# Optimization experiments

Hardware: AMD Instinct MI355X
Metric: run time of the kernel (lower is better)

Reference implementation:

```python
import jax, jax.numpy as jnp
import numpy as np

N_NODES = 50000
N_EDGES = 800000
D = 64            # NODE_FEATURE_DIM == EDGE_FEATURE_DIM
H = 128           # EDGE_FEATURE_HIDDEN
EDGE_STEPS = 4
NODE_STEPS = 2


def _mlp2(h, W1, b1, W2, b2):
    # two-layer MLP with ReLU between (bn=False, end_with_relu=False)
    return jnp.maximum(h @ W1 + b1, 0.0) @ W2 + b2


def setup_inputs() -> dict:
    key = jax.random.key(0)
    ks = iter(jax.random.split(key, 40))

    def w(shape):
        fan_in = shape[0]
        return jax.random.normal(next(ks), shape, dtype=jnp.float32) / np.sqrt(fan_in)

    inp = {
        "x": jax.random.normal(next(ks), (N_NODES, 128), dtype=jnp.float32),
        "edge_attr": jax.random.normal(next(ks), (N_EDGES, 19), dtype=jnp.float32),
        "edge_index": jax.random.randint(next(ks), (2, N_EDGES), 0, N_NODES),
        "node_types": jax.random.randint(next(ks), (N_NODES,), 0, 17),
        # node embedding MLP: 128 -> 64 -> 64
        "ne_W1": w((128, D)), "ne_b1": jnp.zeros((D,)), "ne_W2": w((D, D)), "ne_b2": jnp.zeros((D,)),
        # edge embedding MLP: 19 -> 64 -> 64
        "ee_W1": w((19, D)), "ee_b1": jnp.zeros((D,)), "ee_W2": w((D, D)), "ee_b2": jnp.zeros((D,)),
        # MPN edge MLP: [x_src(2D), x_dst(2D), e(2D)] = 384 -> 128 -> 64
        "mp_eW1": w((6 * D, H)), "mp_eb1": jnp.zeros((H,)), "mp_eW2": w((H, D)), "mp_eb2": jnp.zeros((D,)),
        # MPN node-update MLP: 64 -> 64
        "mp_nW": w((D, D)), "mp_nb": jnp.zeros((D,)),
        # edge classification head: 64 -> 32 -> 1
        "ec_W1": w((D, 32)), "ec_b1": jnp.zeros((32,)), "ec_W2": w((32, 1)), "ec_b2": jnp.zeros((1,)),
        # node classification head: 64 -> 32 -> 1
        "nc_W1": w((D, 32)), "nc_b1": jnp.zeros((32,)), "nc_W2": w((32, 1)), "nc_b2": jnp.zeros((1,)),
        # type classification head: 64 -> 32 -> 17
        "cl_W1": w((D, 32)), "cl_b1": jnp.zeros((32,)), "cl_W2": w((32, 17)), "cl_b2": jnp.zeros((17,)),
    }
    return inp


def reference(x, edge_attr, edge_index, node_types,
              ne_W1, ne_b1, ne_W2, ne_b2,
              ee_W1, ee_b1, ee_W2, ee_b2,
              mp_eW1, mp_eb1, mp_eW2, mp_eb2,
              mp_nW, mp_nb,
              ec_W1, ec_b1, ec_W2, ec_b2,
              nc_W1, nc_b1, nc_W2, nc_b2,
              cl_W1, cl_b1, cl_W2, cl_b2):
    src, dst = edge_index[0], edge_index[1]

    nf0 = _mlp2(x, ne_W1, ne_b1, ne_W2, ne_b2)          # [N, D] initial node emb
    ef0 = _mlp2(edge_attr, ee_W1, ee_b1, ee_W2, ee_b2)  # [E, D] initial edge emb
    nf, ef = nf0, ef0

    def mpn_step(nf, ef):
        # skip connections: concat initial features each iteration
        nf_c = jnp.concatenate([nf0, nf], axis=1)   # [N, 2D]
        ef_c = jnp.concatenate([ef0, ef], axis=1)   # [E, 2D]
        msg_in = jnp.concatenate([nf_c[src], nf_c[dst], ef_c], axis=1)  # [E, 6D]
        e_new = _mlp2(msg_in, mp_eW1, mp_eb1, mp_eW2, mp_eb2)           # [E, D]
        agg = jax.ops.segment_sum(e_new, dst, num_segments=N_NODES)    # [N, D]
        n_new = jnp.maximum(agg @ mp_nW + mp_nb, 0.0)                   # [N, D]
        return n_new, e_new

    for _ in range(EDGE_STEPS):
        nf, ef = mpn_step(nf, ef)
    pred_edge = _mlp2(ef, ec_W1, ec_b1, ec_W2, ec_b2).squeeze(-1)  # [E]

    for _ in range(NODE_STEPS):
        nf, ef = mpn_step(nf, ef)
    pred_node = _mlp2(nf, nc_W1, nc_b1, nc_W2, nc_b2).squeeze(-1)  # [N]
    pred_class = _mlp2(nf, cl_W1, cl_b1, cl_W2, cl_b2)             # [N, 17]

    return (pred_edge, pred_node, pred_class)
```

## Files before the change

kernel.cpp:

```cpp
#include <hip/hip_runtime.h>

#define NN 50000
#define EE 800000

typedef unsigned short u16;
typedef __attribute__((ext_vector_type(8))) short bf16x8;
typedef __attribute__((ext_vector_type(4))) float f32x4;

#define MFMA16(a, b, c) __builtin_amdgcn_mfma_f32_16x16x32_bf16(a, b, c, 0, 0, 0)

__device__ __forceinline__ float bf2f(u16 v) {
    union { unsigned u; float f; } x; x.u = ((unsigned)v) << 16; return x.f;
}
__device__ __forceinline__ u16 f2bf(float f) {
    union { float f; unsigned u; } x; x.f = f;
    unsigned r = x.u + 0x7FFFu + ((x.u >> 16) & 1u);
    return (u16)(r >> 16);
}
__device__ __forceinline__ void gl_lds16(const u16* g, u16* l) {
    __builtin_amdgcn_global_load_lds((const __attribute__((address_space(1))) void*)g,
                                     (__attribute__((address_space(3))) void*)l, 16, 0, 0);
}

__global__ void pack_frag(const float* __restrict__ W, u16* __restrict__ dst, int K, int N) {
    int i = blockIdx.x * 256 + threadIdx.x;
    int nfc = N / 16, kkc = (K + 31) / 32;
    int total = kkc * nfc * 512;
    if (i >= total) return;
    int t = i & 7, lane = (i >> 3) & 63;
    int rest = i >> 9;
    int nf = rest % nfc, kk = rest / nfc;
    int k = kk * 32 + (lane >> 4) * 8 + t, n = nf * 16 + (lane & 15);
    dst[i] = (k < K) ? f2bf(W[k * N + n]) : (u16)0;
}

__global__ __launch_bounds__(256) void embed_mfma_node(
    const float* __restrict__ x, const u16* __restrict__ pW1, const float* __restrict__ b1,
    const u16* __restrict__ pW2, const float* __restrict__ b2, u16* __restrict__ out)
{
    __shared__ alignas(16) u16 A[64 * 136];
    __shared__ alignas(16) u16 Hs[64 * 72];
    int tid = threadIdx.x;
    size_t row0 = (size_t)blockIdx.x * 64;
    #pragma unroll
    for (int it = 0; it < 8; ++it) {
        int u = it * 256 + tid;
        int row = u >> 5, seg = u & 31;
        float4 v = (row0 + row < NN) ? *(const float4*)(x + (row0 + row) * 128 + seg * 4)
                                     : make_float4(0.f, 0.f, 0.f, 0.f);
        ushort4 o; o.x = f2bf(v.x); o.y = f2bf(v.y); o.z = f2bf(v.z); o.w = f2bf(v.w);
        *(ushort4*)(A + row * 136 + seg * 4) = o;
    }
    __syncthreads();
    int wave = tid >> 6, lane = tid & 63, l15 = lane & 15, l4 = lane >> 4;
    int col = wave * 16 + l15;
    f32x4 acc[4] = {};
    #pragma unroll
    for (int kk = 0; kk < 4; ++kk) {
        bf16x8 b = *(const bf16x8*)(pW1 + (size_t)((kk * 4 + wave) * 64 + lane) * 8);
        #pragma unroll
        for (int mi = 0; mi < 4; ++mi) {
            bf16x8 a = *(const bf16x8*)(A + (mi * 16 + l15) * 136 + kk * 32 + l4 * 8);
            acc[mi] = MFMA16(a, b, acc[mi]);
        }
    }
    float bias = b1[col];
    #pragma unroll
    for (int mi = 0; mi < 4; ++mi)
        #pragma unroll
        for (int r = 0; r < 4; ++r) {
            float v = acc[mi][r] + bias;
            Hs[(mi * 16 + l4 * 4 + r) * 72 + col] = f2bf(v > 0.f ? v : 0.f);
        }
    __syncthreads();
    f32x4 acc2[4] = {};
    #pragma unroll
    for (int kk = 0; kk < 2; ++kk) {
        bf16x8 b = *(const bf16x8*)(pW2 + (size_t)((kk * 4 + wave) * 64 + lane) * 8);
        #pragma unroll
        for (int mi = 0; mi < 4; ++mi) {
            bf16x8 a = *(const bf16x8*)(Hs + (mi * 16 + l15) * 72 + kk * 32 + l4 * 8);
            acc2[mi] = MFMA16(a, b, acc2[mi]);
        }
    }
    float bias2 = b2[col];
    __syncthreads();
    #pragma unroll
    for (int mi = 0; mi < 4; ++mi)
        #pragma unroll
        for (int r = 0; r < 4; ++r)
            Hs[(mi * 16 + l4 * 4 + r) * 72 + col] = f2bf(acc2[mi][r] + bias2);
    __syncthreads();
    #pragma unroll
    for (int it = 0; it < 4; ++it) {
        int u = it * 256 + tid;
        int row = u >> 4, c4 = (u & 15) * 4;
        if (row0 + row < NN) {
            ushort4 o = *(const ushort4*)(Hs + row * 72 + c4);
            *(ushort4*)(out + (row0 + row) * 64 + c4) = o;
        }
    }
}

__global__ __launch_bounds__(256) void embed_mfma_edge(
    const float* __restrict__ ea, const u16* __restrict__ pW1, const float* __restrict__ b1,
    const u16* __restrict__ pW2, const float* __restrict__ b2, u16* __restrict__ out)
{
    __shared__ alignas(16) u16 A[64 * 40];
    __shared__ alignas(16) u16 Hs[64 * 72];
    int tid = threadIdx.x;
    size_t row0 = (size_t)blockIdx.x * 64;
    #pragma unroll
    for (int it = 0; it < 8; ++it) {
        int u = it * 256 + tid;
        int row = u >> 5, k = u & 31;
        float v = (k < 19) ? ea[(row0 + row) * 19 + k] : 0.f;
        A[row * 40 + k] = f2bf(v);
    }
    __syncthreads();
    int wave = tid >> 6, lane = tid & 63, l15 = lane & 15, l4 = lane >> 4;
    int col = wave * 16 + l15;
    f32x4 acc[4] = {};
    {
        bf16x8 b = *(const bf16x8*)(pW1 + (size_t)(wave * 64 + lane) * 8);
        #pragma unroll
        for (int mi = 0; mi < 4; ++mi) {
            bf16x8 a = *(const bf16x8*)(A + (mi * 16 + l15) * 40 + l4 * 8);
            acc[mi] = MFMA16(a, b, acc[mi]);
        }
    }
    float bias = b1[col];
    #pragma unroll
    for (int mi = 0; mi < 4; ++mi)
        #pragma unroll
        for (int r = 0; r < 4; ++r) {
            float v = acc[mi][r] + bias;
            Hs[(mi * 16 + l4 * 4 + r) * 72 + col] = f2bf(v > 0.f ? v : 0.f);
        }
    __syncthreads();
    f32x4 acc2[4] = {};
    #pragma unroll
    for (int kk = 0; kk < 2; ++kk) {
        bf16x8 b = *(const bf16x8*)(pW2 + (size_t)((kk * 4 + wave) * 64 + lane) * 8);
        #pragma unroll
        for (int mi = 0; mi < 4; ++mi) {
            bf16x8 a = *(const bf16x8*)(Hs + (mi * 16 + l15) * 72 + kk * 32 + l4 * 8);
            acc2[mi] = MFMA16(a, b, acc2[mi]);
        }
    }
    float bias2 = b2[col];
    __syncthreads();
    #pragma unroll
    for (int mi = 0; mi < 4; ++mi)
        #pragma unroll
        for (int r = 0; r < 4; ++r)
            Hs[(mi * 16 + l4 * 4 + r) * 72 + col] = f2bf(acc2[mi][r] + bias2);
    __syncthreads();
    #pragma unroll
    for (int it = 0; it < 4; ++it) {
        int u = it * 256 + tid;
        int row = u >> 4, c4 = (u & 15) * 4;
        ushort4 o = *(const ushort4*)(Hs + row * 72 + c4);
        *(ushort4*)(out + (row0 + row) * 64 + c4) = o;
    }
}

__global__ void zero_cnt(int* __restrict__ cnt) {
    int i = blockIdx.x * 256 + threadIdx.x;
    if (i < NN) cnt[i] = 0;
}
__global__ void count_deg(const int* __restrict__ eidx, int* __restrict__ cnt) {
    int e = blockIdx.x * 256 + threadIdx.x;
    if (e < EE) atomicAdd(&cnt[eidx[EE + e]], 1);
}
__global__ void scan_k(const int* __restrict__ cnt, int* __restrict__ starts) {
    __shared__ int part[1024];
    int t = threadIdx.x;
    const int chunk = (NN + 1023) / 1024;
    int lo = t * chunk, hi = lo + chunk; if (hi > NN) hi = NN;
    if (lo > NN) lo = NN;
    int s = 0;
    for (int i = lo; i < hi; ++i) s += cnt[i];
    part[t] = s;
    __syncthreads();
    for (int off = 1; off < 1024; off <<= 1) {
        int v = part[t];
        int add = (t >= off) ? part[t - off] : 0;
        __syncthreads();
        part[t] = v + add;
        __syncthreads();
    }
    int run = (t == 0) ? 0 : part[t - 1];
    for (int i = lo; i < hi; ++i) { starts[i] = run; run += cnt[i]; }
    if (t == 1023) starts[NN] = EE;
}
__global__ void init_cur(const int* __restrict__ starts, int* __restrict__ cur) {
    int i = blockIdx.x * 256 + threadIdx.x;
    if (i < NN) cur[i] = starts[i];
}
__global__ void scatter_e(const int* __restrict__ eidx, int* __restrict__ cur,
                          int* __restrict__ eids) {
    int e = blockIdx.x * 256 + threadIdx.x;
    if (e < EE) {
        int pos = atomicAdd(&cur[eidx[EE + e]], 1);
        eids[pos] = e;
    }
}

__global__ __launch_bounds__(256, 3) void edge_mlp(
    const int* __restrict__ eidx,
    const u16* __restrict__ nf0, const u16* __restrict__ nfc,
    const u16* __restrict__ ef0, const u16* __restrict__ efc,
    const u16* __restrict__ pW1, const u16* __restrict__ pW2,
    const float* __restrict__ eb1, const float* __restrict__ eb2,
    u16* __restrict__ efn)
{
    __shared__ alignas(16) u16 Chunk[6][64 * 64];
    const int tid = threadIdx.x;
    const int tile0 = blockIdx.x * 64;
    const int wave = tid >> 6, lane = tid & 63;
    const int l15 = lane & 15, l4 = lane >> 4;

    const int r0 = wave * 16 + (lane >> 3);
    const int r1 = r0 + 8;
    const int u_ = lane & 7;
    const int su0 = u_ ^ (r0 & 7);
    const int su1 = u_ ^ (r1 & 7);
    const int is0 = eidx[tile0 + r0] * 64;
    const int is1 = eidx[tile0 + r1] * 64;
    const int id0 = eidx[EE + tile0 + r0] * 64;
    const int id1 = eidx[EE + tile0 + r1] * 64;

    bf16x8 bw[24];
    #pragma unroll
    for (int kk = 0; kk < 12; ++kk) {
        bw[kk * 2 + 0] = *(const bf16x8*)(pW1 + (size_t)((kk * 8 + wave * 2 + 0) * 64 + lane) * 8);
        bw[kk * 2 + 1] = *(const bf16x8*)(pW1 + (size_t)((kk * 8 + wave * 2 + 1) * 64 + lane) * 8);
    }
    __builtin_amdgcn_sched_barrier(0);

    #pragma unroll
    for (int c = 0; c < 6; ++c) {
        const u16 *b0, *b1;
        if (c == 0)      { b0 = nf0 + is0; b1 = nf0 + is1; }
        else if (c == 1) { b0 = nfc + is0; b1 = nfc + is1; }
        else if (c == 2) { b0 = nf0 + id0; b1 = nf0 + id1; }
        else if (c == 3) { b0 = nfc + id0; b1 = nfc + id1; }
        else if (c == 4) { b0 = ef0 + (size_t)(tile0 + r0) * 64; b1 = ef0 + (size_t)(tile0 + r1) * 64; }
        else             { b0 = efc + (size_t)(tile0 + r0) * 64; b1 = efc + (size_t)(tile0 + r1) * 64; }
        u16* l0 = (u16*)Chunk + c * 4096 + wave * 1024;
        gl_lds16(b0 + su0 * 8, l0);
        gl_lds16(b1 + su1 * 8, l0 + 512);
    }
    __builtin_amdgcn_sched_barrier(0);

    f32x4 acc[4][2] = {};
    #pragma unroll
    for (int c = 0; c < 6; ++c) {
        if (c == 0)      asm volatile("s_waitcnt vmcnt(10)" ::: "memory");
        else if (c == 1) asm volatile("s_waitcnt vmcnt(8)" ::: "memory");
        else if (c == 2) asm volatile("s_waitcnt vmcnt(6)" ::: "memory");
        else if (c == 3) asm volatile("s_waitcnt vmcnt(4)" ::: "memory");
        else if (c == 4) asm volatile("s_waitcnt vmcnt(2)" ::: "memory");
        else             asm volatile("s_waitcnt vmcnt(0)" ::: "memory");
        __builtin_amdgcn_s_barrier();
        __builtin_amdgcn_sched_barrier(0);
        const char* Cb = (const char*)Chunk + c * 8192;
        #pragma unroll
        for (int kkl = 0; kkl < 2; ++kkl) {
            const int kk = c * 2 + kkl;
            #pragma unroll
            for (int mi = 0; mi < 4; ++mi) {
                int row = mi * 16 + l15;
                bf16x8 a = *(const bf16x8*)(Cb + row * 128 + ((kkl * 64 + l4 * 16) ^ ((row & 7) << 4)));
                acc[mi][0] = MFMA16(a, bw[kk * 2 + 0], acc[mi][0]);
                acc[mi][1] = MFMA16(a, bw[kk * 2 + 1], acc[mi][1]);
            }
        }
    }

    char* HidB = (char*)Chunk;
    #pragma unroll
    for (int nj = 0; nj < 2; ++nj) {
        int col = wave * 32 + nj * 16 + l15;
        float bias = eb1[col];
        #pragma unroll
        for (int mi = 0; mi < 4; ++mi) {
            #pragma unroll
            for (int r = 0; r < 4; ++r) {
                int row = mi * 16 + l4 * 4 + r;
                float v = acc[mi][nj][r] + bias;
                v = v > 0.f ? v : 0.f;
                *(u16*)(HidB + row * 256 + ((col * 2) ^ ((row & 7) << 4))) = f2bf(v);
            }
        }
    }
    __syncthreads();

    f32x4 acc2[4] = {};
    const int m0 = wave * 16;
    #pragma unroll
    for (int kk = 0; kk < 4; ++kk) {
        int row = m0 + l15;
        bf16x8 a = *(const bf16x8*)(HidB + row * 256 + ((kk * 64 + l4 * 16) ^ ((row & 7) << 4)));
        #pragma unroll
        for (int nf = 0; nf < 4; ++nf) {
            bf16x8 b = *(const bf16x8*)(pW2 + (size_t)((kk * 4 + nf) * 64 + lane) * 8);
            acc2[nf] = MFMA16(a, b, acc2[nf]);
        }
    }

    float* EnF = (float*)((char*)Chunk + 16384);
    #pragma unroll
    for (int nf = 0; nf < 4; ++nf) {
        int col = nf * 16 + l15;
        float bias = eb2[col];
        #pragma unroll
        for (int r = 0; r < 4; ++r) {
            int row = m0 + l4 * 4 + r;
            EnF[row * 64 + col] = acc2[nf][r] + bias;
        }
    }
    __syncthreads();
    #pragma unroll
    for (int rep = 0; rep < 4; ++rep) {
        int u = rep * 256 + tid;
        int el = u >> 4, d0 = (u & 15) * 4;
        const float* s = EnF + el * 64 + d0;
        ushort4 o;
        o.x = f2bf(s[0]); o.y = f2bf(s[1]); o.z = f2bf(s[2]); o.w = f2bf(s[3]);
        *(ushort4*)(efn + (size_t)(tile0 + el) * 64 + d0) = o;
    }
}

__global__ __launch_bounds__(256) void node_update(
    const u16* __restrict__ enew,
    const int* __restrict__ starts, const int* __restrict__ eids,
    const float* __restrict__ Wn, const float* __restrict__ bn,
    u16* __restrict__ nfn)
{
    __shared__ float Wns[64 * 64];
    int tid = threadIdx.x;
    for (int i = tid; i < 4096; i += 256) Wns[i] = Wn[i];
    __syncthreads();
    int w = tid >> 6, l = tid & 63, g = l >> 4, q = l & 15;
    int nbase = blockIdx.x * 64 + w * 16;
    float bnl = bn[l];
    for (int ni = 0; ni < 16; ++ni) {
        int n = nbase + ni;
        if (n >= NN) break;
        int s0 = starts[n], s1 = starts[n + 1];
        float a0 = 0.f, a1 = 0.f, a2 = 0.f, a3 = 0.f;
        for (int j0 = s0; j0 < s1; j0 += 4) {
            int j = j0 + g;
            if (j < s1) {
                int e = eids[j];
                ushort4 v = *(const ushort4*)(enew + (size_t)e * 64 + q * 4);
                a0 += bf2f(v.x); a1 += bf2f(v.y); a2 += bf2f(v.z); a3 += bf2f(v.w);
            }
        }
        a0 += __shfl_xor(a0, 16); a0 += __shfl_xor(a0, 32);
        a1 += __shfl_xor(a1, 16); a1 += __shfl_xor(a1, 32);
        a2 += __shfl_xor(a2, 16); a2 += __shfl_xor(a2, 32);
        a3 += __shfl_xor(a3, 16); a3 += __shfl_xor(a3, 32);
        float o = bnl;
        #pragma unroll
        for (int hq = 0; hq < 16; ++hq) {
            float b0 = __shfl(a0, hq), b1 = __shfl(a1, hq);
            float b2 = __shfl(a2, hq), b3 = __shfl(a3, hq);
            o += b0 * Wns[(hq * 4 + 0) * 64 + l];
            o += b1 * Wns[(hq * 4 + 1) * 64 + l];
            o += b2 * Wns[(hq * 4 + 2) * 64 + l];
            o += b3 * Wns[(hq * 4 + 3) * 64 + l];
        }
        o = o > 0.f ? o : 0.f;
        nfn[(size_t)n * 64 + l] = f2bf(o);
    }
}

__global__ __launch_bounds__(256) void edge_head(
    const u16* __restrict__ ef, const u16* __restrict__ pW1, const float* __restrict__ b1,
    const float* __restrict__ W2, const float* __restrict__ b2, float* __restrict__ out)
{
    __shared__ alignas(16) u16 A[64 * 72];
    int tid = threadIdx.x;
    int tile0 = blockIdx.x * 64;
    #pragma unroll
    for (int it = 0; it < 2; ++it) {
        int u = it * 256 + tid;
        int row = u >> 3, sub = u & 7;
        uint4 v = *(const uint4*)(ef + (size_t)(tile0 + row) * 64 + sub * 8);
        *(uint4*)(A + row * 72 + sub * 8) = v;
    }
    __syncthreads();
    int wave = tid >> 6, lane = tid & 63, l15 = lane & 15, l4 = lane >> 4;
    int m0 = wave * 16;
    f32x4 acc[2] = {};
    #pragma unroll
    for (int kk = 0; kk < 2; ++kk) {
        bf16x8 a = *(const bf16x8*)(A + (m0 + l15) * 72 + kk * 32 + l4 * 8);
        #pragma unroll
        for (int nf = 0; nf < 2; ++nf) {
            bf16x8 b = *(const bf16x8*)(pW1 + (size_t)((kk * 2 + nf) * 64 + lane) * 8);
            acc[nf] = MFMA16(a, b, acc[nf]);
        }
    }
    float bias2 = b2[0];
    #pragma unroll
    for (int r = 0; r < 4; ++r) {
        float p = 0.f;
        #pragma unroll
        for (int nf = 0; nf < 2; ++nf) {
            int col = nf * 16 + l15;
            float h = acc[nf][r] + b1[col];
            p += (h > 0.f ? h : 0.f) * W2[col];
        }
        p += __shfl_xor(p, 1); p += __shfl_xor(p, 2);
        p += __shfl_xor(p, 4); p += __shfl_xor(p, 8);
        if (l15 == 0) out[tile0 + m0 + l4 * 4 + r] = p + bias2;
    }
}

__global__ void node_head(const u16* __restrict__ nf,
                          const float* __restrict__ ncW1, const float* __restrict__ ncb1,
                          const float* __restrict__ ncW2, const float* __restrict__ ncb2,
                          const float* __restrict__ clW1, const float* __restrict__ clb1,
                          const float* __restrict__ clW2, const float* __restrict__ clb2,
                          float* __restrict__ outN, float* __restrict__ outC) {
    __shared__ float sNW1[2048], sCW1[2048], sCW2[32 * 17];
    __shared__ float sNb1[32], sCb1[32], sNW2[32], sCb2[17];
    int tid = threadIdx.x;
    for (int i = tid; i < 2048; i += 256) { sNW1[i] = ncW1[i]; sCW1[i] = clW1[i]; }
    for (int i = tid; i < 544; i += 256) sCW2[i] = clW2[i];
    if (tid < 32) { sNb1[tid] = ncb1[tid]; sCb1[tid] = clb1[tid]; sNW2[tid] = ncW2[tid]; }
    if (tid < 17) sCb2[tid] = clb2[tid];
    __syncthreads();
    int n = blockIdx.x * 256 + tid;
    if (n >= NN) return;
    const u16* r = nf + (size_t)n * 64;
    float v[64];
    for (int k4 = 0; k4 < 16; ++k4) {
        ushort4 q = *(const ushort4*)(r + k4 * 4);
        v[k4 * 4 + 0] = bf2f(q.x); v[k4 * 4 + 1] = bf2f(q.y);
        v[k4 * 4 + 2] = bf2f(q.z); v[k4 * 4 + 3] = bf2f(q.w);
    }
    float h[32];
    #pragma unroll
    for (int j = 0; j < 32; ++j) h[j] = sNb1[j];
    for (int k = 0; k < 64; ++k) {
        float vk = v[k];
        #pragma unroll
        for (int j = 0; j < 32; ++j) h[j] += vk * sNW1[k * 32 + j];
    }
    float o = ncb2[0];
    #pragma unroll
    for (int j = 0; j < 32; ++j) o += (h[j] > 0.f ? h[j] : 0.f) * sNW2[j];
    outN[n] = o;
    #pragma unroll
    for (int j = 0; j < 32; ++j) h[j] = sCb1[j];
    for (int k = 0; k < 64; ++k) {
        float vk = v[k];
        #pragma unroll
        for (int j = 0; j < 32; ++j) h[j] += vk * sCW1[k * 32 + j];
    }
    float oc[17];
    #pragma unroll
    for (int c = 0; c < 17; ++c) oc[c] = sCb2[c];
    #pragma unroll
    for (int j = 0; j < 32; ++j) {
        float hr = h[j] > 0.f ? h[j] : 0.f;
        #pragma unroll
        for (int c = 0; c < 17; ++c) oc[c] += hr * sCW2[j * 17 + c];
    }
    #pragma unroll
    for (int c = 0; c < 17; ++c) outC[(size_t)n * 17 + c] = oc[c];
}

extern "C" void kernel_launch(void* const* d_in, const int* in_sizes, int n_in,
                              void* d_out, int out_size, void* d_ws, size_t ws_size,
                              hipStream_t stream) {
    const float* x     = (const float*)d_in[0];
    const float* ea    = (const float*)d_in[1];
    const int*   eidx  = (const int*)d_in[2];
    const float* neW1  = (const float*)d_in[4];
    const float* neb1  = (const float*)d_in[5];
    const float* neW2  = (const float*)d_in[6];
    const float* neb2  = (const float*)d_in[7];
    const float* eeW1  = (const float*)d_in[8];
    const float* eeb1  = (const float*)d_in[9];
    const float* eeW2  = (const float*)d_in[10];
    const float* eeb2  = (const float*)d_in[11];
    const float* mpW1  = (const float*)d_in[12];
    const float* mpb1  = (const float*)d_in[13];
    const float* mpW2  = (const float*)d_in[14];
    const float* mpb2  = (const float*)d_in[15];
    const float* mpnW  = (const float*)d_in[16];
    const float* mpnb  = (const float*)d_in[17];
    const float* ecW1  = (const float*)d_in[18];
    const float* ecb1  = (const float*)d_in[19];
    const float* ecW2  = (const float*)d_in[20];
    const float* ecb2  = (const float*)d_in[21];
    const float* ncW1  = (const float*)d_in[22];
    const float* ncb1  = (const float*)d_in[23];
    const float* ncW2  = (const float*)d_in[24];
    const float* ncb2  = (const float*)d_in[25];
    const float* clW1  = (const float*)d_in[26];
    const float* clb1  = (const float*)d_in[27];
    const float* clW2  = (const float*)d_in[28];
    const float* clb2  = (const float*)d_in[29];

    char* w = (char*)d_ws;
    size_t used = 0;
    auto alloc = [&](size_t b) {
        char* p = w + used; used += (b + 255) & ~(size_t)255; return p;
    };
    u16* nf0  = (u16*)alloc((size_t)NN * 64 * 2);
    u16* nfW  = (u16*)alloc((size_t)NN * 64 * 2);
    u16* ef0  = (u16*)alloc((size_t)EE * 64 * 2);
    u16* efW  = (u16*)alloc((size_t)EE * 64 * 2);
    u16* pmW1 = (u16*)alloc(49152 * 2);
    u16* pmW2 = (u16*)alloc(8192 * 2);
    u16* pnW1 = (u16*)alloc(8192 * 2);
    u16* pnW2 = (u16*)alloc(4096 * 2);
    u16* peW1 = (u16*)alloc(2048 * 2);
    u16* peW2 = (u16*)alloc(4096 * 2);
    u16* pcW1 = (u16*)alloc(2048 * 2);
    int* cnt    = (int*)alloc((size_t)NN * 4);
    int* starts = (int*)alloc((size_t)(NN + 1) * 4);
    int* eids   = (int*)alloc((size_t)EE * 4);
    if (used > ws_size) return;

    pack_frag<<<192, 256, 0, stream>>>(mpW1, pmW1, 384, 128);
    pack_frag<<<32, 256, 0, stream>>>(mpW2, pmW2, 128, 64);
    pack_frag<<<32, 256, 0, stream>>>(neW1, pnW1, 128, 64);
    pack_frag<<<16, 256, 0, stream>>>(neW2, pnW2, 64, 64);
    pack_frag<<<8, 256, 0, stream>>>(eeW1, peW1, 19, 64);
    pack_frag<<<16, 256, 0, stream>>>(eeW2, peW2, 64, 64);
    pack_frag<<<8, 256, 0, stream>>>(ecW1, pcW1, 64, 32);

    embed_mfma_node<<<(NN + 63) / 64, 256, 0, stream>>>(x, pnW1, neb1, pnW2, neb2, nf0);
    embed_mfma_edge<<<EE / 64, 256, 0, stream>>>(ea, peW1, eeb1, peW2, eeb2, ef0);

    zero_cnt<<<(NN + 255) / 256, 256, 0, stream>>>(cnt);
    count_deg<<<EE / 256, 256, 0, stream>>>(eidx, cnt);
    scan_k<<<1, 1024, 0, stream>>>(cnt, starts);
    init_cur<<<(NN + 255) / 256, 256, 0, stream>>>(starts, cnt);
    scatter_e<<<EE / 256, 256, 0, stream>>>(eidx, cnt, eids);

    float* outE = (float*)d_out;
    float* outN = outE + EE;
    float* outC = outN + NN;

    const u16* nfc = nf0;
    const u16* efc = ef0;
    for (int s = 0; s < 6; ++s) {
        edge_mlp<<<EE / 64, 256, 0, stream>>>(eidx, nf0, nfc, ef0, efc, pmW1, pmW2, mpb1, mpb2, efW);
        node_update<<<(NN + 63) / 64, 256, 0, stream>>>(efW, starts, eids, mpnW, mpnb, nfW);
        if (s == 3)
            edge_head<<<EE / 64, 256, 0, stream>>>(efW, pcW1, ecb1, ecW2, ecb2, outE);
        efc = efW;
        nfc = nfW;
    }
    node_head<<<(NN + 255) / 256, 256, 0, stream>>>(nfc, ncW1, ncb1, ncW2, ncb2,
                                                    clW1, clb1, clW2, clb2, outN, outC);
    (void)in_sizes; (void)n_in; (void)out_size;
}
```

Before: 1.533 ms.

## Shrink edge_mlp LDS to five chunks and restructure node_update gather

edge_mlp now stages five 64x64 input chunks instead of six. After the first chunk has been consumed, its buffer is reused for the efc chunk, which brings LDS use down to 40KB and raises the occupancy hint from 3 to 4 blocks per CU. node_update moves from one node per wave to one node per 16-lane group. Each lane loads edge ids cooperatively, the ids are broadcast with shuffles, and gathers are unrolled four at a time; the 64x64 projection uses float4 weights and 4 outputs per lane. The goal is more latency hiding and memory-level parallelism. The cost is an extra barrier and a serialized refill in edge_mlp, plus possible load imbalance across nodes of different degree.

```diff
diff --git a/kernel.cpp b/kernel.cpp
--- a/kernel.cpp
+++ b/kernel.cpp
@@ -207,7 +207,7 @@
     }
 }
 
-__global__ __launch_bounds__(256, 3) void edge_mlp(
+__global__ __launch_bounds__(256, 4) void edge_mlp(
     const int* __restrict__ eidx,
     const u16* __restrict__ nf0, const u16* __restrict__ nfc,
     const u16* __restrict__ ef0, const u16* __restrict__ efc,
@@ -215,7 +215,7 @@
     const float* __restrict__ eb1, const float* __restrict__ eb2,
     u16* __restrict__ efn)
 {
-    __shared__ alignas(16) u16 Chunk[6][64 * 64];
+    __shared__ alignas(16) u16 Chunk[5][64 * 64];
     const int tid = threadIdx.x;
     const int tile0 = blockIdx.x * 64;
     const int wave = tid >> 6, lane = tid & 63;
@@ -240,14 +240,13 @@
     __builtin_amdgcn_sched_barrier(0);
 
     #pragma unroll
-    for (int c = 0; c < 6; ++c) {
+    for (int c = 0; c < 5; ++c) {
         const u16 *b0, *b1;
         if (c == 0)      { b0 = nf0 + is0; b1 = nf0 + is1; }
         else if (c == 1) { b0 = nfc + is0; b1 = nfc + is1; }
         else if (c == 2) { b0 = nf0 + id0; b1 = nf0 + id1; }
         else if (c == 3) { b0 = nfc + id0; b1 = nfc + id1; }
-        else if (c == 4) { b0 = ef0 + (size_t)(tile0 + r0) * 64; b1 = ef0 + (size_t)(tile0 + r1) * 64; }
-        else             { b0 = efc + (size_t)(tile0 + r0) * 64; b1 = efc + (size_t)(tile0 + r1) * 64; }
+        else             { b0 = ef0 + (size_t)(tile0 + r0) * 64; b1 = ef0 + (size_t)(tile0 + r1) * 64; }
         u16* l0 = (u16*)Chunk + c * 4096 + wave * 1024;
         gl_lds16(b0 + su0 * 8, l0);
         gl_lds16(b1 + su1 * 8, l0 + 512);
@@ -255,31 +254,56 @@
     __builtin_amdgcn_sched_barrier(0);
 
     f32x4 acc[4][2] = {};
-    #pragma unroll
-    for (int c = 0; c < 6; ++c) {
-        if (c == 0)      asm volatile("s_waitcnt vmcnt(10)" ::: "memory");
-        else if (c == 1) asm volatile("s_waitcnt vmcnt(8)" ::: "memory");
-        else if (c == 2) asm volatile("s_waitcnt vmcnt(6)" ::: "memory");
-        else if (c == 3) asm volatile("s_waitcnt vmcnt(4)" ::: "memory");
-        else if (c == 4) asm volatile("s_waitcnt vmcnt(2)" ::: "memory");
-        else             asm volatile("s_waitcnt vmcnt(0)" ::: "memory");
-        __builtin_amdgcn_s_barrier();
-        __builtin_amdgcn_sched_barrier(0);
-        const char* Cb = (const char*)Chunk + c * 8192;
+    auto gemm_chunk = [&](int buf, int kk0) {
+        const char* Cb = (const char*)Chunk + buf * 8192;
         #pragma unroll
         for (int kkl = 0; kkl < 2; ++kkl) {
-            const int kk = c * 2 + kkl;
             #pragma unroll
             for (int mi = 0; mi < 4; ++mi) {
                 int row = mi * 16 + l15;
                 bf16x8 a = *(const bf16x8*)(Cb + row * 128 + ((kkl * 64 + l4 * 16) ^ ((row & 7) << 4)));
-                acc[mi][0] = MFMA16(a, bw[kk * 2 + 0], acc[mi][0]);
-                acc[mi][1] = MFMA16(a, bw[kk * 2 + 1], acc[mi][1]);
+                acc[mi][0] = MFMA16(a, bw[(kk0 + kkl) * 2 + 0], acc[mi][0]);
+                acc[mi][1] = MFMA16(a, bw[(kk0 + kkl) * 2 + 1], acc[mi][1]);
             }
         }
-    }
-
-    char* HidB = (char*)Chunk;
+    };
+
+    asm volatile("s_waitcnt vmcnt(8)" ::: "memory");
+    __builtin_amdgcn_s_barrier();
+    __builtin_amdgcn_sched_barrier(0);
+    gemm_chunk(0, 0);
+    __builtin_amdgcn_s_barrier();
+    __builtin_amdgcn_sched_barrier(0);
+    {
+        const u16* b0 = efc + (size_t)(tile0 + r0) * 64;
+        const u16* b1 = efc + (size_t)(tile0 + r1) * 64;
+        u16* l0 = (u16*)Chunk + wave * 1024;
+        gl_lds16(b0 + su0 * 8, l0);
+        gl_lds16(b1 + su1 * 8, l0 + 512);
+    }
+    __builtin_amdgcn_sched_barrier(0);
+    asm volatile("s_waitcnt vmcnt(8)" ::: "memory");
+    __builtin_amdgcn_s_barrier();
+    __builtin_amdgcn_sched_barrier(0);
+    gemm_chunk(1, 2);
+    asm volatile("s_waitcnt vmcnt(6)" ::: "memory");
+    __builtin_amdgcn_s_barrier();
+    __builtin_amdgcn_sched_barrier(0);
+    gemm_chunk(2, 4);
+    asm volatile("s_waitcnt vmcnt(4)" ::: "memory");
+    __builtin_amdgcn_s_barrier();
+    __builtin_amdgcn_sched_barrier(0);
+    gemm_chunk(3, 6);
+    asm volatile("s_waitcnt vmcnt(2)" ::: "memory");
+    __builtin_amdgcn_s_barrier();
+    __builtin_amdgcn_sched_barrier(0);
+    gemm_chunk(4, 8);
+    asm volatile("s_waitcnt vmcnt(0)" ::: "memory");
+    __builtin_amdgcn_s_barrier();
+    __builtin_amdgcn_sched_barrier(0);
+    gemm_chunk(0, 10);
+
+    char* HidB = (char*)Chunk + 8192;
     #pragma unroll
     for (int nj = 0; nj < 2; ++nj) {
         int col = wave * 32 + nj * 16 + l15;
@@ -310,7 +334,7 @@
         }
     }
 
-    float* EnF = (float*)((char*)Chunk + 16384);
+    float* EnF = (float*)((char*)Chunk + 24576);
     #pragma unroll
     for (int nf = 0; nf < 4; ++nf) {
         int col = nf * 16 + l15;
@@ -343,39 +367,60 @@
     int tid = threadIdx.x;
     for (int i = tid; i < 4096; i += 256) Wns[i] = Wn[i];
     __syncthreads();
-    int w = tid >> 6, l = tid & 63, g = l >> 4, q = l & 15;
-    int nbase = blockIdx.x * 64 + w * 16;
-    float bnl = bn[l];
-    for (int ni = 0; ni < 16; ++ni) {
-        int n = nbase + ni;
-        if (n >= NN) break;
-        int s0 = starts[n], s1 = starts[n + 1];
-        float a0 = 0.f, a1 = 0.f, a2 = 0.f, a3 = 0.f;
-        for (int j0 = s0; j0 < s1; j0 += 4) {
-            int j = j0 + g;
-            if (j < s1) {
-                int e = eids[j];
-                ushort4 v = *(const ushort4*)(enew + (size_t)e * 64 + q * 4);
-                a0 += bf2f(v.x); a1 += bf2f(v.y); a2 += bf2f(v.z); a3 += bf2f(v.w);
-            }
-        }
-        a0 += __shfl_xor(a0, 16); a0 += __shfl_xor(a0, 32);
-        a1 += __shfl_xor(a1, 16); a1 += __shfl_xor(a1, 32);
-        a2 += __shfl_xor(a2, 16); a2 += __shfl_xor(a2, 32);
-        a3 += __shfl_xor(a3, 16); a3 += __shfl_xor(a3, 32);
-        float o = bnl;
-        #pragma unroll
-        for (int hq = 0; hq < 16; ++hq) {
-            float b0 = __shfl(a0, hq), b1 = __shfl(a1, hq);
-            float b2 = __shfl(a2, hq), b3 = __shfl(a3, hq);
-            o += b0 * Wns[(hq * 4 + 0) * 64 + l];
-            o += b1 * Wns[(hq * 4 + 1) * 64 + l];
-            o += b2 * Wns[(hq * 4 + 2) * 64 + l];
-            o += b3 * Wns[(hq * 4 + 3) * 64 + l];
-        }
-        o = o > 0.f ? o : 0.f;
-        nfn[(size_t)n * 64 + l] = f2bf(o);
-    }
+    const int l = tid & 63;
+    const int q = l & 15;
+    const int base = l & 48;
+    const int n = blockIdx.x * 16 + (tid >> 4);
+    if (n >= NN) return;
+    const int s0 = starts[n], s1 = starts[n + 1];
+    float a0 = 0.f, a1 = 0.f, a2 = 0.f, a3 = 0.f;
+    for (int j0 = s0; j0 < s1; j0 += 16) {
+        int jj = j0 + q;
+        int e = (jj < s1) ? eids[jj] : 0;
+        int cnt = s1 - j0; if (cnt > 16) cnt = 16;
+        int i = 0;
+        for (; i + 4 <= cnt; i += 4) {
+            int e0 = __shfl(e, base | (i + 0));
+            int e1 = __shfl(e, base | (i + 1));
+            int e2 = __shfl(e, base | (i + 2));
+            int e3 = __shfl(e, base | (i + 3));
+            ushort4 v0 = *(const ushort4*)(enew + (size_t)e0 * 64 + q * 4);
+            ushort4 v1 = *(const ushort4*)(enew + (size_t)e1 * 64 + q * 4);
+            ushort4 v2 = *(const ushort4*)(enew + (size_t)e2 * 64 + q * 4);
+            ushort4 v3 = *(const ushort4*)(enew + (size_t)e3 * 64 + q * 4);
+            a0 += bf2f(v0.x) + bf2f(v1.x) + bf2f(v2.x) + bf2f(v3.x);
+            a1 += bf2f(v0.y) + bf2f(v1.y) + bf2f(v2.y) + bf2f(v3.y);
+            a2 += bf2f(v0.z) + bf2f(v1.z) + bf2f(v2.z) + bf2f(v3.z);
+            a3 += bf2f(v0.w) + bf2f(v1.w) + bf2f(v2.w) + bf2f(v3.w);
+        }
+        for (; i < cnt; ++i) {
+            int e0 = __shfl(e, base | i);
+            ushort4 v0 = *(const ushort4*)(enew + (size_t)e0 * 64 + q * 4);
+            a0 += bf2f(v0.x); a1 += bf2f(v0.y); a2 += bf2f(v0.z); a3 += bf2f(v0.w);
+        }
+    }
+    const float4 bb = *(const float4*)(bn + q * 4);
+    float o0 = bb.x, o1 = bb.y, o2 = bb.z, o3 = bb.w;
+    #pragma unroll
+    for (int hq = 0; hq < 16; ++hq) {
+        int src = base | hq;
+        float b0 = __shfl(a0, src), b1 = __shfl(a1, src);
+        float b2 = __shfl(a2, src), b3 = __shfl(a3, src);
+        const float4 w0 = *(const float4*)(Wns + (hq * 4 + 0) * 64 + q * 4);
+        const float4 w1 = *(const float4*)(Wns + (hq * 4 + 1) * 64 + q * 4);
+        const float4 w2 = *(const float4*)(Wns + (hq * 4 + 2) * 64 + q * 4);
+        const float4 w3 = *(const float4*)(Wns + (hq * 4 + 3) * 64 + q * 4);
+        o0 += b0 * w0.x + b1 * w1.x + b2 * w2.x + b3 * w3.x;
+        o1 += b0 * w0.y + b1 * w1.y + b2 * w2.y + b3 * w3.y;
+        o2 += b0 * w0.z + b1 * w1.z + b2 * w2.z + b3 * w3.z;
+        o3 += b0 * w0.w + b1 * w1.w + b2 * w2.w + b3 * w3.w;
+    }
+    ushort4 o;
+    o.x = f2bf(o0 > 0.f ? o0 : 0.f);
+    o.y = f2bf(o1 > 0.f ? o1 : 0.f);
+    o.z = f2bf(o2 > 0.f ? o2 : 0.f);
+    o.w = f2bf(o3 > 0.f ? o3 : 0.f);
+    *(ushort4*)(nfn + (size_t)n * 64 + q * 4) = o;
 }
 
 __global__ __launch_bounds__(256) void edge_head(
@@ -555,7 +600,7 @@
     const u16* efc = ef0;
     for (int s = 0; s < 6; ++s) {
         edge_mlp<<<EE / 64, 256, 0, stream>>>(eidx, nf0, nfc, ef0, efc, pmW1, pmW2, mpb1, mpb2, efW);
-        node_update<<<(NN + 63) / 64, 256, 0, stream>>>(efW, starts, eids, mpnW, mpnb, nfW);
+        node_update<<<(NN + 15) / 16, 256, 0, stream>>>(efW, starts, eids, mpnW, mpnb, nfW);
         if (s == 3)
             edge_head<<<EE / 64, 256, 0, stream>>>(efW, pcW1, ecb1, ecW2, ecb2, outE);
         efc = efW;
```

New measurement: 1.527 ms. Within noise of the previous version (-0.4%).

## Store edges in destination-sorted order to make segment sum contiguous

Applied to the files above, without the earlier changes.

Permutes all edge feature arrays into CSR (destination-sorted) order: the edge embedding gathers raw attributes through eids, the edge MLP reads permuted src/dst index arrays, and the edge head scatters its outputs back to the original edge order. Node aggregation then reads each node's incoming edges as one contiguous run instead of indirecting through eids. This also gives destination-node gathers in the edge MLP better locality. Node update is remapped to 16 lanes per node with vectorized weight reads, and an empty asm pins the preloaded weight registers. Costs are an extra permutation kernel, two index arrays, and a scattered write in the edge head.

```diff
diff --git a/kernel.cpp b/kernel.cpp
--- a/kernel.cpp
+++ b/kernel.cpp
@@ -103,18 +103,22 @@
 }
 
 __global__ __launch_bounds__(256) void embed_mfma_edge(
-    const float* __restrict__ ea, const u16* __restrict__ pW1, const float* __restrict__ b1,
+    const float* __restrict__ ea, const int* __restrict__ eids,
+    const u16* __restrict__ pW1, const float* __restrict__ b1,
     const u16* __restrict__ pW2, const float* __restrict__ b2, u16* __restrict__ out)
 {
     __shared__ alignas(16) u16 A[64 * 40];
     __shared__ alignas(16) u16 Hs[64 * 72];
+    __shared__ int eid_s[64];
     int tid = threadIdx.x;
     size_t row0 = (size_t)blockIdx.x * 64;
+    if (tid < 64) eid_s[tid] = eids[row0 + tid];
+    __syncthreads();
     #pragma unroll
     for (int it = 0; it < 8; ++it) {
         int u = it * 256 + tid;
         int row = u >> 5, k = u & 31;
-        float v = (k < 19) ? ea[(row0 + row) * 19 + k] : 0.f;
+        float v = (k < 19) ? ea[(size_t)eid_s[row] * 19 + k] : 0.f;
         A[row * 40 + k] = f2bf(v);
     }
     __syncthreads();
@@ -206,9 +210,18 @@
         eids[pos] = e;
     }
 }
+__global__ void build_perm(const int* __restrict__ eidx, const int* __restrict__ eids,
+                           int* __restrict__ psrc, int* __restrict__ pdst) {
+    int j = blockIdx.x * 256 + threadIdx.x;
+    if (j < EE) {
+        int e = eids[j];
+        psrc[j] = eidx[e];
+        pdst[j] = eidx[EE + e];
+    }
+}
 
 __global__ __launch_bounds__(256, 3) void edge_mlp(
-    const int* __restrict__ eidx,
+    const int* __restrict__ psrc, const int* __restrict__ pdst,
     const u16* __restrict__ nf0, const u16* __restrict__ nfc,
     const u16* __restrict__ ef0, const u16* __restrict__ efc,
     const u16* __restrict__ pW1, const u16* __restrict__ pW2,
@@ -226,10 +239,10 @@
     const int u_ = lane & 7;
     const int su0 = u_ ^ (r0 & 7);
     const int su1 = u_ ^ (r1 & 7);
-    const int is0 = eidx[tile0 + r0] * 64;
-    const int is1 = eidx[tile0 + r1] * 64;
-    const int id0 = eidx[EE + tile0 + r0] * 64;
-    const int id1 = eidx[EE + tile0 + r1] * 64;
+    const int is0 = psrc[tile0 + r0] * 64;
+    const int is1 = psrc[tile0 + r1] * 64;
+    const int id0 = pdst[tile0 + r0] * 64;
+    const int id1 = pdst[tile0 + r1] * 64;
 
     bf16x8 bw[24];
     #pragma unroll
@@ -237,6 +250,8 @@
         bw[kk * 2 + 0] = *(const bf16x8*)(pW1 + (size_t)((kk * 8 + wave * 2 + 0) * 64 + lane) * 8);
         bw[kk * 2 + 1] = *(const bf16x8*)(pW1 + (size_t)((kk * 8 + wave * 2 + 1) * 64 + lane) * 8);
     }
+    #pragma unroll
+    for (int i = 0; i < 24; ++i) asm volatile("" : "+v"(bw[i]));
     __builtin_amdgcn_sched_barrier(0);
 
     #pragma unroll
@@ -334,8 +349,8 @@
 }
 
 __global__ __launch_bounds__(256) void node_update(
-    const u16* __restrict__ enew,
-    const int* __restrict__ starts, const int* __restrict__ eids,
+    const u16* __restrict__ enewp,
+    const int* __restrict__ starts,
     const float* __restrict__ Wn, const float* __restrict__ bn,
     u16* __restrict__ nfn)
 {
@@ -343,43 +358,57 @@
     int tid = threadIdx.x;
     for (int i = tid; i < 4096; i += 256) Wns[i] = Wn[i];
     __syncthreads();
-    int w = tid >> 6, l = tid & 63, g = l >> 4, q = l & 15;
-    int nbase = blockIdx.x * 64 + w * 16;
-    float bnl = bn[l];
-    for (int ni = 0; ni < 16; ++ni) {
-        int n = nbase + ni;
-        if (n >= NN) break;
-        int s0 = starts[n], s1 = starts[n + 1];
-        float a0 = 0.f, a1 = 0.f, a2 = 0.f, a3 = 0.f;
-        for (int j0 = s0; j0 < s1; j0 += 4) {
-            int j = j0 + g;
-            if (j < s1) {
-                int e = eids[j];
-                ushort4 v = *(const ushort4*)(enew + (size_t)e * 64 + q * 4);
-                a0 += bf2f(v.x); a1 += bf2f(v.y); a2 += bf2f(v.z); a3 += bf2f(v.w);
-            }
-        }
-        a0 += __shfl_xor(a0, 16); a0 += __shfl_xor(a0, 32);
-        a1 += __shfl_xor(a1, 16); a1 += __shfl_xor(a1, 32);
-        a2 += __shfl_xor(a2, 16); a2 += __shfl_xor(a2, 32);
-        a3 += __shfl_xor(a3, 16); a3 += __shfl_xor(a3, 32);
-        float o = bnl;
-        #pragma unroll
-        for (int hq = 0; hq < 16; ++hq) {
-            float b0 = __shfl(a0, hq), b1 = __shfl(a1, hq);
-            float b2 = __shfl(a2, hq), b3 = __shfl(a3, hq);
-            o += b0 * Wns[(hq * 4 + 0) * 64 + l];
-            o += b1 * Wns[(hq * 4 + 1) * 64 + l];
-            o += b2 * Wns[(hq * 4 + 2) * 64 + l];
-            o += b3 * Wns[(hq * 4 + 3) * 64 + l];
-        }
-        o = o > 0.f ? o : 0.f;
-        nfn[(size_t)n * 64 + l] = f2bf(o);
-    }
+    const int l = tid & 63;
+    const int q = l & 15;
+    const int base = l & 48;
+    const int n = blockIdx.x * 16 + (tid >> 4);
+    if (n >= NN) return;
+    const int s0 = starts[n], s1 = starts[n + 1];
+    const int cnt = s1 - s0;
+    const u16* p = enewp + (size_t)s0 * 64 + q * 4;
+    float a0 = 0.f, a1 = 0.f, a2 = 0.f, a3 = 0.f;
+    int i = 0;
+    for (; i + 4 <= cnt; i += 4) {
+        ushort4 v0 = *(const ushort4*)(p + (i + 0) * 64);
+        ushort4 v1 = *(const ushort4*)(p + (i + 1) * 64);
+        ushort4 v2 = *(const ushort4*)(p + (i + 2) * 64);
+        ushort4 v3 = *(const ushort4*)(p + (i + 3) * 64);
+        a0 += bf2f(v0.x) + bf2f(v1.x) + bf2f(v2.x) + bf2f(v3.x);
+        a1 += bf2f(v0.y) + bf2f(v1.y) + bf2f(v2.y) + bf2f(v3.y);
+        a2 += bf2f(v0.z) + bf2f(v1.z) + bf2f(v2.z) + bf2f(v3.z);
+        a3 += bf2f(v0.w) + bf2f(v1.w) + bf2f(v2.w) + bf2f(v3.w);
+    }
+    for (; i < cnt; ++i) {
+        ushort4 v0 = *(const ushort4*)(p + i * 64);
+        a0 += bf2f(v0.x); a1 += bf2f(v0.y); a2 += bf2f(v0.z); a3 += bf2f(v0.w);
+    }
+    const float4 bb = *(const float4*)(bn + q * 4);
+    float o0 = bb.x, o1 = bb.y, o2 = bb.z, o3 = bb.w;
+    #pragma unroll
+    for (int hq = 0; hq < 16; ++hq) {
+        int src = base | hq;
+        float b0 = __shfl(a0, src), b1 = __shfl(a1, src);
+        float b2 = __shfl(a2, src), b3 = __shfl(a3, src);
+        const float4 w0 = *(const float4*)(Wns + (hq * 4 + 0) * 64 + q * 4);
+        const float4 w1 = *(const float4*)(Wns + (hq * 4 + 1) * 64 + q * 4);
+        const float4 w2 = *(const float4*)(Wns + (hq * 4 + 2) * 64 + q * 4);
+        const float4 w3 = *(const float4*)(Wns + (hq * 4 + 3) * 64 + q * 4);
+        o0 += b0 * w0.x + b1 * w1.x + b2 * w2.x + b3 * w3.x;
+        o1 += b0 * w0.y + b1 * w1.y + b2 * w2.y + b3 * w3.y;
+        o2 += b0 * w0.z + b1 * w1.z + b2 * w2.z + b3 * w3.z;
+        o3 += b0 * w0.w + b1 * w1.w + b2 * w2.w + b3 * w3.w;
+    }
+    ushort4 o;
+    o.x = f2bf(o0 > 0.f ? o0 : 0.f);
+    o.y = f2bf(o1 > 0.f ? o1 : 0.f);
+    o.z = f2bf(o2 > 0.f ? o2 : 0.f);
+    o.w = f2bf(o3 > 0.f ? o3 : 0.f);
+    *(ushort4*)(nfn + (size_t)n * 64 + q * 4) = o;
 }
 
 __global__ __launch_bounds__(256) void edge_head(
-    const u16* __restrict__ ef, const u16* __restrict__ pW1, const float* __restrict__ b1,
+    const u16* __restrict__ ef, const int* __restrict__ eids,
+    const u16* __restrict__ pW1, const float* __restrict__ b1,
     const float* __restrict__ W2, const float* __restrict__ b2, float* __restrict__ out)
 {
     __shared__ alignas(16) u16 A[64 * 72];
@@ -417,7 +446,7 @@
         }
         p += __shfl_xor(p, 1); p += __shfl_xor(p, 2);
         p += __shfl_xor(p, 4); p += __shfl_xor(p, 8);
-        if (l15 == 0) out[tile0 + m0 + l4 * 4 + r] = p + bias2;
+        if (l15 == 0) out[eids[tile0 + m0 + l4 * 4 + r]] = p + bias2;
     }
 }
 
@@ -528,6 +557,8 @@
     int* cnt    = (int*)alloc((size_t)NN * 4);
     int* starts = (int*)alloc((size_t)(NN + 1) * 4);
     int* eids   = (int*)alloc((size_t)EE * 4);
+    int* psrc   = (int*)alloc((size_t)EE * 4);
+    int* pdst   = (int*)alloc((size_t)EE * 4);
     if (used > ws_size) return;
 
     pack_frag<<<192, 256, 0, stream>>>(mpW1, pmW1, 384, 128);
@@ -538,14 +569,15 @@
     pack_frag<<<16, 256, 0, stream>>>(eeW2, peW2, 64, 64);
     pack_frag<<<8, 256, 0, stream>>>(ecW1, pcW1, 64, 32);
 
-    embed_mfma_node<<<(NN + 63) / 64, 256, 0, stream>>>(x, pnW1, neb1, pnW2, neb2, nf0);
-    embed_mfma_edge<<<EE / 64, 256, 0, stream>>>(ea, peW1, eeb1, peW2, eeb2, ef0);
-
     zero_cnt<<<(NN + 255) / 256, 256, 0, stream>>>(cnt);
     count_deg<<<EE / 256, 256, 0, stream>>>(eidx, cnt);
     scan_k<<<1, 1024, 0, stream>>>(cnt, starts);
     init_cur<<<(NN + 255) / 256, 256, 0, stream>>>(starts, cnt);
     scatter_e<<<EE / 256, 256, 0, stream>>>(eidx, cnt, eids);
+    build_perm<<<EE / 256, 256, 0, stream>>>(eidx, eids, psrc, pdst);
+
+    embed_mfma_node<<<(NN + 63) / 64, 256, 0, stream>>>(x, pnW1, neb1, pnW2, neb2, nf0);
+    embed_mfma_edge<<<EE / 64, 256, 0, stream>>>(ea, eids, peW1, eeb1, peW2, eeb2, ef0);
 
     float* outE = (float*)d_out;
     float* outN = outE + EE;
@@ -554,10 +586,11 @@
     const u16* nfc = nf0;
     const u16* efc = ef0;
     for (int s = 0; s < 6; ++s) {
-        edge_mlp<<<EE / 64, 256, 0, stream>>>(eidx, nf0, nfc, ef0, efc, pmW1, pmW2, mpb1, mpb2, efW);
-        node_update<<<(NN + 63) / 64, 256, 0, stream>>>(efW, starts, eids, mpnW, mpnb, nfW);
+        edge_mlp<<<EE / 64, 256, 0, stream>>>(psrc, pdst, nf0, nfc, ef0, efc,
+                                              pmW1, pmW2, mpb1, mpb2, efW);
+        node_update<<<(NN + 15) / 16, 256, 0, stream>>>(efW, starts, mpnW, mpnb, nfW);
         if (s == 3)
-            edge_head<<<EE / 64, 256, 0, stream>>>(efW, pcW1, ecb1, ecW2, ecb2, outE);
+            edge_head<<<EE / 64, 256, 0, stream>>>(efW, eids, pcW1, ecb1, ecW2, ecb2, outE);
         efc = efW;
         nfc = nfW;
     }
```

Result: faster. 1.238 ms (-19.2%).
